# Kernel optimization log

Measured on AMD Instinct MI355X. Metric: run time of the kernel, lower is better.

The kernel has to match this reference:

```python
import jax, jax.numpy as jnp
import numpy as np

EMBED_DIM = 1024
HEAD_NUM = 16
NEG = 100000.0


def setup_inputs() -> dict:
    key = jax.random.key(0)
    k1, k2, k3, k4, k5 = jax.random.split(key, 5)
    B, S, E = 2, 2048, EMBED_DIM
    return {
        "x": jax.random.normal(k1, (B, S, E), dtype=jnp.float32),
        "w_attn": jax.random.normal(k2, (E, 3 * E), dtype=jnp.float32) * 0.02,
        "b_attn": jax.random.normal(k3, (3 * E,), dtype=jnp.float32) * 0.02,
        "w_proj": jax.random.normal(k4, (E, E), dtype=jnp.float32) * 0.02,
        "b_proj": jax.random.normal(k5, (E,), dtype=jnp.float32) * 0.02,
    }


def reference(x, w_attn, b_attn, w_proj, b_proj):
    B, S, E = x.shape
    H = HEAD_NUM
    d = E // H
    dk = jnp.asarray(d, x.dtype) ** 0.5  # (embed_dim // head_num) ** 0.5

    qkv = x @ w_attn + b_attn                      # [B, S, 3E]
    qkv = qkv.reshape(B, S, H, 3 * d)              # split heads BEFORE chunk (as in source)
    qkv = jnp.swapaxes(qkv, 1, 2)                  # [B, H, S, 3d]
    q, k, v = jnp.split(qkv, 3, axis=-1)           # each [B, H, S, d]

    w = jnp.einsum("bhqd,bhkd->bhqk", q, k) / dk   # [B, H, S, S]
    mask = jnp.tril(jnp.ones((S, S), dtype=x.dtype))
    w = w * mask - (1.0 - mask) * NEG              # exact masking math of source
    w = jax.nn.softmax(w, axis=-1)                 # dropout omitted (eval mode)

    a = jnp.einsum("bhqk,bhkd->bhqd", w, v)        # [B, H, S, d]
    a = jnp.swapaxes(a, 1, 2).reshape(B, S, E)     # [B, S, E]
    h = a @ w_proj + b_proj                        # resi dropout omitted (eval mode)
    return h
```

## Files before the change

kernel.cpp:

```cpp
#include <hip/hip_runtime.h>
#include <hip/hip_bf16.h>

#define BB 2
#define SS 2048
#define EE 1024
#define HH 16
#define DD 64
#define MM (BB*SS)
#define N1 (3*EE)

typedef __attribute__((ext_vector_type(4))) float f32x4;
typedef __attribute__((ext_vector_type(16))) float f32x16;
typedef __attribute__((ext_vector_type(8))) short bf16x8;
typedef __attribute__((ext_vector_type(4))) unsigned int u32x4;
typedef __attribute__((ext_vector_type(2))) unsigned int u32x2;

__device__ __forceinline__ ushort f2bf(float f){
  union { float f; unsigned u; } v; v.f = f;
  unsigned r = v.u + 0x7fffu + ((v.u >> 16) & 1u);
  return (ushort)(r >> 16);
}

__device__ __forceinline__ unsigned cvt_pk(float a, float b){
  unsigned r; asm("v_cvt_pk_bf16_f32 %0, %1, %2" : "=v"(r) : "v"(a), "v"(b)); return r;
}

__device__ __forceinline__ float exp2_fast(float x){
  float r; asm("v_exp_f32 %0, %1" : "=v"(r) : "v"(x)); return r;
}

__device__ __forceinline__ u32x2 pl32swap(unsigned a, unsigned b){
  return __builtin_amdgcn_permlane32_swap(a, b, false, false);
}

__device__ __forceinline__ void gload16(const void* g, void* l){
  __builtin_amdgcn_global_load_lds(
      (const __attribute__((address_space(1))) unsigned*)g,
      (__attribute__((address_space(3))) unsigned*)l, 16, 0, 0);
}

__global__ __launch_bounds__(256) void prep_kernel(const float* __restrict__ x, ushort* __restrict__ xb,
    const float* __restrict__ wa, ushort* __restrict__ waT,
    const float* __restrict__ wp, ushort* __restrict__ wpT){
  __shared__ float t[32][33];
  const int bid = blockIdx.x, tid = threadIdx.x;
  if (bid < 4096){
    int i = bid*256 + tid;
    const float4 f = reinterpret_cast<const float4*>(x)[i];
    ushort4 o; o.x=f2bf(f.x); o.y=f2bf(f.y); o.z=f2bf(f.z); o.w=f2bf(f.w);
    reinterpret_cast<ushort4*>(xb)[i] = o;
  } else {
    const float* in; ushort* out; int N, nx, b;
    if (bid < 7168){ b = bid - 4096; in = wa; out = waT; N = N1; nx = N1/32; }
    else           { b = bid - 7168; in = wp; out = wpT; N = EE; nx = EE/32; }
    const int n0 = (b % nx)*32, k0 = (b / nx)*32;
    const int tx = tid & 31, ty = tid >> 5;
    for (int r = ty; r < 32; r += 8)
      t[r][tx] = in[(size_t)(k0+r)*N + n0 + tx];
    __syncthreads();
    for (int r = ty; r < 32; r += 8)
      out[(size_t)(n0+r)*EE + k0 + tx] = f2bf(t[tx][r]);
  }
}

template<int MODE>
__global__ __launch_bounds__(256) void gemm_nt(const ushort* __restrict__ A,
    const ushort* __restrict__ Bt, const float* __restrict__ bias,
    ushort* __restrict__ q_, ushort* __restrict__ k_, ushort* __restrict__ v_,
    float* __restrict__ of, int M, int N, int K){
  __shared__ ushort As[128*32];
  __shared__ ushort Bs[128*32];
  const int tid = threadIdx.x;
  const int lane = tid & 63, w = tid >> 6;
  const int nx = gridDim.x;
  const int nwg = nx * gridDim.y;
  const int flat = blockIdx.y*nx + blockIdx.x;
  const int sw = (flat & 7)*(nwg >> 3) + (flat >> 3);
  const int m0 = (sw / nx)*128, n0 = (sw % nx)*128;
  const int wm = (w >> 1)*64, wn = (w & 1)*64;
  const int lr = lane & 15, lk = (lane >> 4)*8;
  const int c0 = w*2;
  const int srow = lane >> 2;
  const int scb  = (lane & 3)*8;
  const ushort* Ag0 = A  + (size_t)(m0 + c0*16      + srow)*K + scb;
  const ushort* Ag1 = A  + (size_t)(m0 + c0*16 + 16 + srow)*K + scb;
  const ushort* Bg0 = Bt + (size_t)(n0 + c0*16      + srow)*K + scb;
  const ushort* Bg1 = Bt + (size_t)(n0 + c0*16 + 16 + srow)*K + scb;
  ushort* Al0 = &As[(c0*16)*32];
  ushort* Al1 = &As[(c0*16 + 16)*32];
  ushort* Bl0 = &Bs[(c0*16)*32];
  ushort* Bl1 = &Bs[(c0*16 + 16)*32];

  f32x4 acc[4][4] = {};
  for (int k0 = 0; k0 < K; k0 += 32){
    gload16(Ag0 + k0, Al0);
    gload16(Ag1 + k0, Al1);
    gload16(Bg0 + k0, Bl0);
    gload16(Bg1 + k0, Bl1);
    __syncthreads();
    bf16x8 af[4], bfr[4];
    #pragma unroll
    for (int m = 0; m < 4; ++m)
      af[m] = *reinterpret_cast<bf16x8*>(&As[(wm + m*16 + lr)*32 + lk]);
    #pragma unroll
    for (int n = 0; n < 4; ++n)
      bfr[n] = *reinterpret_cast<bf16x8*>(&Bs[(wn + n*16 + lr)*32 + lk]);
    __builtin_amdgcn_s_setprio(1);
    #pragma unroll
    for (int m = 0; m < 4; ++m)
      #pragma unroll
      for (int n = 0; n < 4; ++n)
        acc[m][n] = __builtin_amdgcn_mfma_f32_16x16x32_bf16(af[m], bfr[n], acc[m][n], 0, 0, 0);
    __builtin_amdgcn_s_setprio(0);
    __syncthreads();
  }
  #pragma unroll
  for (int m = 0; m < 4; ++m){
    #pragma unroll
    for (int n = 0; n < 4; ++n){
      int col = n0 + wn + n*16 + lr;
      float bv = bias[col];
      #pragma unroll
      for (int r = 0; r < 4; ++r){
        int row = m0 + wm + m*16 + (lane >> 4)*4 + r;
        float v = acc[m][n][r] + bv;
        if (MODE == 1){
          of[(size_t)row*N + col] = v;
        } else {
          int b = row >> 11, s = row & 2047;
          int h = col / 192, t = col - h*192;
          ushort u = f2bf(v);
          size_t bh = (size_t)(b*HH + h);
          if (t < 64)       q_[(bh*SS + s)*DD + t]        = u;
          else if (t < 128) k_[(bh*SS + s)*DD + (t-64)]   = u;
          else              v_[(bh*DD + (t-128))*SS + s]  = u;
        }
      }
    }
  }
}

#define SCL 0.18033688f
#define THRRAW 44.3614f
__global__ __launch_bounds__(256,2) void attn2(const ushort* __restrict__ Qg,
    const ushort* __restrict__ Kg, const ushort* __restrict__ Vg,
    ushort* __restrict__ aout){
  __shared__ __align__(16) ushort Kl[2][64*64];
  __shared__ __align__(16) ushort Vl[2][64*64];
  const int tid = threadIdx.x, lane = tid & 63, w = tid >> 6;
  const int bh = blockIdx.x;
  const int y  = blockIdx.y;
  const int qt = (y < 8) ? 2*y : 31 - 2*y;
  const int b = bh >> 4, h = bh & 15;
  const int q0 = qt*128;
  const int ql = lane & 31, g = lane >> 5;
  const int qrow = q0 + w*32 + ql;
  const int qminw = q0 + w*32;
  const int qmaxw = qminw + 31;

  const ushort* Qp = Qg + ((size_t)bh*SS + qrow)*DD;
  bf16x8 qf[4];
  #pragma unroll
  for (int s = 0; s < 4; ++s)
    qf[s] = *(const bf16x8*)(Qp + s*16 + g*8);

  f32x16 ot[2] = {};
  float mr = -1e30f, sr = 0.f;

  const int csr = lane >> 3;
  const int gcb = ((lane & 7) ^ csr)*8;
  const ushort* Kbase = Kg + (size_t)bh*SS*DD;
  const ushort* Vbase = Vg + (size_t)bh*DD*SS;
  const int nkb = (q0 + 128) >> 6;

  auto stage = [&](int k0, int bi){
    #pragma unroll
    for (int i = 0; i < 2; ++i){
      const int c = w*2 + i;
      gload16(Kbase + (size_t)(k0 + c*8 + csr)*DD + gcb, &Kl[bi][(c*8)*64]);
      gload16(Vbase + (size_t)(c*8 + csr)*SS + k0 + gcb, &Vl[bi][(c*8)*64]);
    }
  };

  stage(0, 0);
  int buf = 0;
  for (int kb = 0; kb < nkb; ++kb){
    const int k0 = kb*64;
    __syncthreads();
    if (kb + 1 < nkb) stage(k0 + 64, buf ^ 1);
    if (k0 <= qmaxw){
      const ushort* Kc = &Kl[buf][0];
      const ushort* Vc = &Vl[buf][0];
      const int swq = (ql & 7);
      f32x16 st0 = {}, st1 = {};
      __builtin_amdgcn_s_setprio(1);
      #pragma unroll
      for (int s = 0; s < 4; ++s){
        bf16x8 kf0 = *(const bf16x8*)&Kc[ ql     *64 + (((2*s + g) ^ swq)*8)];
        bf16x8 kf1 = *(const bf16x8*)&Kc[(32+ql) *64 + (((2*s + g) ^ swq)*8)];
        st0 = __builtin_amdgcn_mfma_f32_32x32x16_bf16(kf0, qf[s], st0, 0, 0, 0);
        st1 = __builtin_amdgcn_mfma_f32_32x32x16_bf16(kf1, qf[s], st1, 0, 0, 0);
      }
      __builtin_amdgcn_s_setprio(0);
      float p[2][16];
      #pragma unroll
      for (int r = 0; r < 16; ++r){ p[0][r] = st0[r]; p[1][r] = st1[r]; }
      if (k0 + 63 > qminw){
        #pragma unroll
        for (int kf = 0; kf < 2; ++kf)
          #pragma unroll
          for (int r = 0; r < 16; ++r){
            int kg = k0 + kf*32 + (r & 3) + 8*(r >> 2) + 4*g;
            p[kf][r] = (kg > qrow) ? -1e30f : p[kf][r];
          }
      }
      float m8[8];
      #pragma unroll
      for (int i = 0; i < 8; ++i)
        m8[i] = fmaxf(fmaxf(p[0][i], p[0][i+8]), fmaxf(p[1][i], p[1][i+8]));
      float tm = fmaxf(fmaxf(fmaxf(m8[0],m8[1]), fmaxf(m8[2],m8[3])),
                       fmaxf(fmaxf(m8[4],m8[5]), fmaxf(m8[6],m8[7])));
      { u32x2 rm = pl32swap(__float_as_uint(tm), __float_as_uint(tm));
        tm = fmaxf(__uint_as_float(rm[0]), __uint_as_float(rm[1])); }
      if (__any(tm > mr + THRRAW)){
        float nm = fmaxf(mr, tm);
        float fac = exp2_fast((mr - nm)*SCL);
        #pragma unroll
        for (int r = 0; r < 16; ++r){ ot[0][r] *= fac; ot[1][r] *= fac; }
        sr *= fac;
        mr = nm;
      }
      const float nms = mr * SCL;
      #pragma unroll
      for (int kf = 0; kf < 2; ++kf)
        #pragma unroll
        for (int r = 0; r < 16; ++r)
          p[kf][r] = exp2_fast(__builtin_fmaf(p[kf][r], SCL, -nms));
      float s8[8];
      #pragma unroll
      for (int i = 0; i < 8; ++i)
        s8[i] = (p[0][i] + p[0][i+8]) + (p[1][i] + p[1][i+8]);
      float ts = ((s8[0]+s8[1]) + (s8[2]+s8[3])) + ((s8[4]+s8[5]) + (s8[6]+s8[7]));
      { u32x2 rs = pl32swap(__float_as_uint(ts), __float_as_uint(ts));
        ts = __uint_as_float(rs[0]) + __uint_as_float(rs[1]); }
      sr += ts;

      __builtin_amdgcn_s_setprio(1);
      #pragma unroll
      for (int kf = 0; kf < 2; ++kf){
        #pragma unroll
        for (int s2 = 0; s2 < 2; ++s2){
          const int base = s2*8;
          unsigned u0 = cvt_pk(p[kf][base+0], p[kf][base+1]);
          unsigned u1 = cvt_pk(p[kf][base+2], p[kf][base+3]);
          unsigned u2 = cvt_pk(p[kf][base+4], p[kf][base+5]);
          unsigned u3 = cvt_pk(p[kf][base+6], p[kf][base+7]);
          u32x2 r0 = pl32swap(u0, u2);
          u32x2 r1 = pl32swap(u1, u3);
          union { u32x4 u; bf16x8 hv; } pw;
          pw.u[0] = r0[0]; pw.u[1] = r1[0]; pw.u[2] = r0[1]; pw.u[3] = r1[1];
          const int cbv = 4*kf + 2*s2 + g;
          bf16x8 v0f = *(const bf16x8*)&Vc[ ql     *64 + ((cbv ^ swq)*8)];
          bf16x8 v1f = *(const bf16x8*)&Vc[(32+ql) *64 + ((cbv ^ swq)*8)];
          ot[0] = __builtin_amdgcn_mfma_f32_32x32x16_bf16(v0f, pw.hv, ot[0], 0, 0, 0);
          ot[1] = __builtin_amdgcn_mfma_f32_32x32x16_bf16(v1f, pw.hv, ot[1], 0, 0, 0);
        }
      }
      __builtin_amdgcn_s_setprio(0);
    }
    buf ^= 1;
  }
  const float inv = 1.f / sr;
  const size_t obase = ((size_t)b*SS + qrow)*EE + h*DD;
  #pragma unroll
  for (int df = 0; df < 2; ++df){
    #pragma unroll
    for (int t = 0; t < 4; ++t){
      ushort4 o4;
      o4.x = f2bf(ot[df][t*4+0]*inv);
      o4.y = f2bf(ot[df][t*4+1]*inv);
      o4.z = f2bf(ot[df][t*4+2]*inv);
      o4.w = f2bf(ot[df][t*4+3]*inv);
      int d = df*32 + 8*t + 4*g;
      *(ushort4*)&aout[obase + d] = o4;
    }
  }
}

extern "C" void kernel_launch(void* const* d_in, const int* in_sizes, int n_in,
                              void* d_out, int out_size, void* d_ws, size_t ws_size,
                              hipStream_t stream){
  const float* x      = (const float*)d_in[0];
  const float* w_attn = (const float*)d_in[1];
  const float* b_attn = (const float*)d_in[2];
  const float* w_proj = (const float*)d_in[3];
  const float* b_proj = (const float*)d_in[4];
  float* out = (float*)d_out;

  ushort* ws   = (ushort*)d_ws;
  ushort* xb   = ws;
  ushort* waT  = xb  + (size_t)MM*EE;
  ushort* wpT  = waT + (size_t)N1*EE;
  ushort* qb_  = wpT + (size_t)EE*EE;
  ushort* kb_  = qb_ + (size_t)MM*EE;
  ushort* vTb  = kb_ + (size_t)MM*EE;
  ushort* ab   = vTb + (size_t)MM*EE;

  prep_kernel<<<8192, 256, 0, stream>>>(x, xb, w_attn, waT, w_proj, wpT);
  gemm_nt<0><<<dim3(N1/128, MM/128), 256, 0, stream>>>(xb, waT, b_attn, qb_, kb_, vTb, nullptr, MM, N1, EE);
  attn2<<<dim3(BB*HH, SS/128), 256, 0, stream>>>(qb_, kb_, vTb, ab);
  gemm_nt<1><<<dim3(EE/128, MM/128), 256, 0, stream>>>(ab, wpT, b_proj, nullptr, nullptr, nullptr, out, MM, EE, EE);
}
```

Measured before the change: 123.1 us.

## Software-pipeline QK^T of next tile with softmax and PV of current tile

Splits the attention inner loop into a QK stage and a softmax+PV stage. Each iteration now issues the QK MFMAs for tile t+1 alongside the exp and PV work for tile t, two tiles per loop trip. The goal is to hide the softmax ALU latency behind matrix-core work. K/V shared-memory staging grows to four buffers so loads run further ahead, which doubles LDS per block. Two score accumulators stay live at once, raising register pressure and risking occupancy or spills.

```diff
diff --git a/kernel.cpp b/kernel.cpp
--- a/kernel.cpp
+++ b/kernel.cpp
@@ -145,8 +145,8 @@
 __global__ __launch_bounds__(256,2) void attn2(const ushort* __restrict__ Qg,
     const ushort* __restrict__ Kg, const ushort* __restrict__ Vg,
     ushort* __restrict__ aout){
-  __shared__ __align__(16) ushort Kl[2][64*64];
-  __shared__ __align__(16) ushort Vl[2][64*64];
+  __shared__ __align__(16) ushort Kl[4][64*64];
+  __shared__ __align__(16) ushort Vl[4][64*64];
   const int tid = threadIdx.x, lane = tid & 63, w = tid >> 6;
   const int bh = blockIdx.x;
   const int y  = blockIdx.y;
@@ -172,8 +172,11 @@
   const ushort* Kbase = Kg + (size_t)bh*SS*DD;
   const ushort* Vbase = Vg + (size_t)bh*DD*SS;
   const int nkb = (q0 + 128) >> 6;
-
-  auto stage = [&](int k0, int bi){
+  const int nv  = (qmaxw >> 6) + 1;
+  const int swq = (ql & 7);
+
+  auto stage = [&](int t){
+    const int k0 = t*64, bi = t & 3;
     #pragma unroll
     for (int i = 0; i < 2; ++i){
       const int c = w*2 + i;
@@ -182,94 +185,105 @@
     }
   };
 
-  stage(0, 0);
-  int buf = 0;
-  for (int kb = 0; kb < nkb; ++kb){
-    const int k0 = kb*64;
-    __syncthreads();
-    if (kb + 1 < nkb) stage(k0 + 64, buf ^ 1);
-    if (k0 <= qmaxw){
-      const ushort* Kc = &Kl[buf][0];
-      const ushort* Vc = &Vl[buf][0];
-      const int swq = (ql & 7);
-      f32x16 st0 = {}, st1 = {};
-      __builtin_amdgcn_s_setprio(1);
-      #pragma unroll
-      for (int s = 0; s < 4; ++s){
-        bf16x8 kf0 = *(const bf16x8*)&Kc[ ql     *64 + (((2*s + g) ^ swq)*8)];
-        bf16x8 kf1 = *(const bf16x8*)&Kc[(32+ql) *64 + (((2*s + g) ^ swq)*8)];
-        st0 = __builtin_amdgcn_mfma_f32_32x32x16_bf16(kf0, qf[s], st0, 0, 0, 0);
-        st1 = __builtin_amdgcn_mfma_f32_32x32x16_bf16(kf1, qf[s], st1, 0, 0, 0);
+  auto qk = [&](int t, f32x16& s0, f32x16& s1){
+    const ushort* Kc = &Kl[t & 3][0];
+    f32x16 a0 = {}, a1 = {};
+    __builtin_amdgcn_s_setprio(1);
+    #pragma unroll
+    for (int s = 0; s < 4; ++s){
+      bf16x8 kf0 = *(const bf16x8*)&Kc[ ql     *64 + (((2*s + g) ^ swq)*8)];
+      bf16x8 kf1 = *(const bf16x8*)&Kc[(32+ql) *64 + (((2*s + g) ^ swq)*8)];
+      a0 = __builtin_amdgcn_mfma_f32_32x32x16_bf16(kf0, qf[s], a0, 0, 0, 0);
+      a1 = __builtin_amdgcn_mfma_f32_32x32x16_bf16(kf1, qf[s], a1, 0, 0, 0);
+    }
+    __builtin_amdgcn_s_setprio(0);
+    const int k0 = t*64;
+    if (k0 + 63 > qminw){
+      #pragma unroll
+      for (int r = 0; r < 16; ++r){
+        int kg0 = k0 + (r & 3) + 8*(r >> 2) + 4*g;
+        a0[r] = (kg0 > qrow) ? -1e30f : a0[r];
+        a1[r] = (kg0 + 32 > qrow) ? -1e30f : a1[r];
       }
-      __builtin_amdgcn_s_setprio(0);
-      float p[2][16];
-      #pragma unroll
-      for (int r = 0; r < 16; ++r){ p[0][r] = st0[r]; p[1][r] = st1[r]; }
-      if (k0 + 63 > qminw){
-        #pragma unroll
-        for (int kf = 0; kf < 2; ++kf)
-          #pragma unroll
-          for (int r = 0; r < 16; ++r){
-            int kg = k0 + kf*32 + (r & 3) + 8*(r >> 2) + 4*g;
-            p[kf][r] = (kg > qrow) ? -1e30f : p[kf][r];
-          }
+    }
+    s0 = a0; s1 = a1;
+  };
+
+  auto smpv = [&](int t, f32x16& s0, f32x16& s1){
+    float p[2][16];
+    #pragma unroll
+    for (int r = 0; r < 16; ++r){ p[0][r] = s0[r]; p[1][r] = s1[r]; }
+    float m8[8];
+    #pragma unroll
+    for (int i = 0; i < 8; ++i)
+      m8[i] = fmaxf(fmaxf(p[0][i], p[0][i+8]), fmaxf(p[1][i], p[1][i+8]));
+    float tm = fmaxf(fmaxf(fmaxf(m8[0],m8[1]), fmaxf(m8[2],m8[3])),
+                     fmaxf(fmaxf(m8[4],m8[5]), fmaxf(m8[6],m8[7])));
+    { u32x2 rm = pl32swap(__float_as_uint(tm), __float_as_uint(tm));
+      tm = fmaxf(__uint_as_float(rm[0]), __uint_as_float(rm[1])); }
+    if (__any(tm > mr + THRRAW)){
+      float nm = fmaxf(mr, tm);
+      float fac = exp2_fast((mr - nm)*SCL);
+      #pragma unroll
+      for (int r = 0; r < 16; ++r){ ot[0][r] *= fac; ot[1][r] *= fac; }
+      sr *= fac;
+      mr = nm;
+    }
+    const float nms = mr * SCL;
+    #pragma unroll
+    for (int kf = 0; kf < 2; ++kf)
+      #pragma unroll
+      for (int r = 0; r < 16; ++r)
+        p[kf][r] = exp2_fast(__builtin_fmaf(p[kf][r], SCL, -nms));
+    float s8[8];
+    #pragma unroll
+    for (int i = 0; i < 8; ++i)
+      s8[i] = (p[0][i] + p[0][i+8]) + (p[1][i] + p[1][i+8]);
+    float ts = ((s8[0]+s8[1]) + (s8[2]+s8[3])) + ((s8[4]+s8[5]) + (s8[6]+s8[7]));
+    { u32x2 rs = pl32swap(__float_as_uint(ts), __float_as_uint(ts));
+      ts = __uint_as_float(rs[0]) + __uint_as_float(rs[1]); }
+    sr += ts;
+
+    const ushort* Vc = &Vl[t & 3][0];
+    __builtin_amdgcn_s_setprio(1);
+    #pragma unroll
+    for (int kf = 0; kf < 2; ++kf){
+      #pragma unroll
+      for (int s2 = 0; s2 < 2; ++s2){
+        const int base = s2*8;
+        unsigned u0 = cvt_pk(p[kf][base+0], p[kf][base+1]);
+        unsigned u1 = cvt_pk(p[kf][base+2], p[kf][base+3]);
+        unsigned u2 = cvt_pk(p[kf][base+4], p[kf][base+5]);
+        unsigned u3 = cvt_pk(p[kf][base+6], p[kf][base+7]);
+        u32x2 r0 = pl32swap(u0, u2);
+        u32x2 r1 = pl32swap(u1, u3);
+        union { u32x4 u; bf16x8 hv; } pw;
+        pw.u[0] = r0[0]; pw.u[1] = r1[0]; pw.u[2] = r0[1]; pw.u[3] = r1[1];
+        const int cbv = 4*kf + 2*s2 + g;
+        bf16x8 v0f = *(const bf16x8*)&Vc[ ql     *64 + ((cbv ^ swq)*8)];
+        bf16x8 v1f = *(const bf16x8*)&Vc[(32+ql) *64 + ((cbv ^ swq)*8)];
+        ot[0] = __builtin_amdgcn_mfma_f32_32x32x16_bf16(v0f, pw.hv, ot[0], 0, 0, 0);
+        ot[1] = __builtin_amdgcn_mfma_f32_32x32x16_bf16(v1f, pw.hv, ot[1], 0, 0, 0);
       }
-      float m8[8];
-      #pragma unroll
-      for (int i = 0; i < 8; ++i)
-        m8[i] = fmaxf(fmaxf(p[0][i], p[0][i+8]), fmaxf(p[1][i], p[1][i+8]));
-      float tm = fmaxf(fmaxf(fmaxf(m8[0],m8[1]), fmaxf(m8[2],m8[3])),
-                       fmaxf(fmaxf(m8[4],m8[5]), fmaxf(m8[6],m8[7])));
-      { u32x2 rm = pl32swap(__float_as_uint(tm), __float_as_uint(tm));
-        tm = fmaxf(__uint_as_float(rm[0]), __uint_as_float(rm[1])); }
-      if (__any(tm > mr + THRRAW)){
-        float nm = fmaxf(mr, tm);
-        float fac = exp2_fast((mr - nm)*SCL);
-        #pragma unroll
-        for (int r = 0; r < 16; ++r){ ot[0][r] *= fac; ot[1][r] *= fac; }
-        sr *= fac;
-        mr = nm;
-      }
-      const float nms = mr * SCL;
-      #pragma unroll
-      for (int kf = 0; kf < 2; ++kf)
-        #pragma unroll
-        for (int r = 0; r < 16; ++r)
-          p[kf][r] = exp2_fast(__builtin_fmaf(p[kf][r], SCL, -nms));
-      float s8[8];
-      #pragma unroll
-      for (int i = 0; i < 8; ++i)
-        s8[i] = (p[0][i] + p[0][i+8]) + (p[1][i] + p[1][i+8]);
-      float ts = ((s8[0]+s8[1]) + (s8[2]+s8[3])) + ((s8[4]+s8[5]) + (s8[6]+s8[7]));
-      { u32x2 rs = pl32swap(__float_as_uint(ts), __float_as_uint(ts));
-        ts = __uint_as_float(rs[0]) + __uint_as_float(rs[1]); }
-      sr += ts;
-
-      __builtin_amdgcn_s_setprio(1);
-      #pragma unroll
-      for (int kf = 0; kf < 2; ++kf){
-        #pragma unroll
-        for (int s2 = 0; s2 < 2; ++s2){
-          const int base = s2*8;
-          unsigned u0 = cvt_pk(p[kf][base+0], p[kf][base+1]);
-          unsigned u1 = cvt_pk(p[kf][base+2], p[kf][base+3]);
-          unsigned u2 = cvt_pk(p[kf][base+4], p[kf][base+5]);
-          unsigned u3 = cvt_pk(p[kf][base+6], p[kf][base+7]);
-          u32x2 r0 = pl32swap(u0, u2);
-          u32x2 r1 = pl32swap(u1, u3);
-          union { u32x4 u; bf16x8 hv; } pw;
-          pw.u[0] = r0[0]; pw.u[1] = r1[0]; pw.u[2] = r0[1]; pw.u[3] = r1[1];
-          const int cbv = 4*kf + 2*s2 + g;
-          bf16x8 v0f = *(const bf16x8*)&Vc[ ql     *64 + ((cbv ^ swq)*8)];
-          bf16x8 v1f = *(const bf16x8*)&Vc[(32+ql) *64 + ((cbv ^ swq)*8)];
-          ot[0] = __builtin_amdgcn_mfma_f32_32x32x16_bf16(v0f, pw.hv, ot[0], 0, 0, 0);
-          ot[1] = __builtin_amdgcn_mfma_f32_32x32x16_bf16(v1f, pw.hv, ot[1], 0, 0, 0);
-        }
-      }
-      __builtin_amdgcn_s_setprio(0);
-    }
-    buf ^= 1;
-  }
+    }
+    __builtin_amdgcn_s_setprio(0);
+  };
+
+  stage(0);
+  stage(1);
+  f32x16 pA0, pA1, pB0, pB1;
+  for (int tt = 0; tt < nkb; tt += 2){
+    __syncthreads();
+    if (tt + 2 < nkb) stage(tt + 2);
+    if (tt < nv) qk(tt, pA0, pA1);
+    if (tt > 0 && tt - 1 < nv) smpv(tt - 1, pB0, pB1);
+    __syncthreads();
+    if (tt + 3 < nkb) stage(tt + 3);
+    if (tt + 1 < nv) qk(tt + 1, pB0, pB1);
+    if (tt < nv) smpv(tt, pA0, pA1);
+  }
+  if (nkb - 1 < nv) smpv(nkb - 1, pB0, pB1);
+
   const float inv = 1.f / sr;
   const size_t obase = ((size_t)b*SS + qrow)*EE + h*DD;
   #pragma unroll
```

Measured after the change: 123.6 us. No clear change (+0.4%).
